# Kernel optimization log

Hardware: AMD Instinct MI355X
Metric: run time of the kernel (lower is better)

The kernel has to match this reference:

```python
import jax, jax.numpy as jnp
import numpy as np

B, T, D, H, E, TOPK = 4, 1024, 1024, 16, 8, 2
DH = D // H
FF = 4 * D
EPS = 1e-9


def setup_inputs() -> dict:
    key = jax.random.key(0)
    ks = jax.random.split(key, 8)
    s = 0.02
    return {
        "x": jax.random.normal(ks[0], (B, T, D), jnp.float32),
        "c": jax.random.normal(ks[1], (B, 1, D), jnp.float32),
        "ln1_w": jnp.ones((D,), jnp.float32),
        "w_qkv": jax.random.normal(ks[2], (3 * D, D), jnp.float32) * s,
        "w_proj": jax.random.normal(ks[3], (D, D), jnp.float32) * s,
        "ln2_w": jnp.ones((D,), jnp.float32),
        "router_w": jax.random.normal(ks[4], (E, D), jnp.float32) * s,
        "expert_w1": jax.random.normal(ks[5], (E, FF, D), jnp.float32) * s,
        "expert_w2": jax.random.normal(ks[6], (E, D, FF), jnp.float32) * s,
    }


def _layernorm(x, w):
    mu = jnp.mean(x, axis=-1, keepdims=True)
    var = jnp.mean(jnp.square(x - mu), axis=-1, keepdims=True)
    return (x - mu) * jax.lax.rsqrt(var + 1e-5) * w


def reference(x, c, ln1_w, w_qkv, w_proj, ln2_w, router_w, expert_w1, expert_w2):
    # --- causal self-attention with AdaLN-style additive conditioning ---
    h = _layernorm(x, ln1_w) + c                          # [B,T,D]
    qkv = jnp.einsum('btd,ed->bte', h, w_qkv)             # [B,T,3D]
    q, k, v = jnp.split(qkv, 3, axis=-1)
    q = q.reshape(B, T, H, DH).transpose(0, 2, 1, 3)       # [B,H,T,dh]
    k = k.reshape(B, T, H, DH).transpose(0, 2, 1, 3)
    v = v.reshape(B, T, H, DH).transpose(0, 2, 1, 3)
    scores = jnp.einsum('bhqd,bhkd->bhqk', q, k) / jnp.sqrt(jnp.float32(DH))
    causal = jnp.tril(jnp.ones((T, T), bool))
    scores = jnp.where(causal, scores, jnp.float32(-1e30))
    attn = jax.nn.softmax(scores, axis=-1)
    o = jnp.einsum('bhqk,bhkd->bhqd', attn, v)
    o = o.transpose(0, 2, 1, 3).reshape(B, T, D)
    x = x + jnp.einsum('btd,ed->bte', o, w_proj)

    # --- pre-MoE LayerNorm (note: module overwrites x with ln_2(x)) ---
    x = _layernorm(x, ln2_w)

    # --- router (non-cond path): linear, max-shift, softmax, eps clamp, top-k ---
    logits = jnp.einsum('btd,ed->bte', x, router_w)        # [B,T,E]
    logits = logits - jnp.max(logits, axis=-1, keepdims=True)
    probs = jax.nn.softmax(logits, axis=-1)
    probs = jnp.clip(probs + EPS, EPS, 1.0 - EPS)
    _, top_idx = jax.lax.top_k(probs, TOPK)                # [B,T,k]
    mask = jnp.sum(jax.nn.one_hot(top_idx, E, dtype=probs.dtype), axis=-2)  # [B,T,E]
    router_probs = mask * probs
    router_probs = router_probs / jnp.sum(router_probs, axis=-1, keepdims=True)

    # --- experts: GPT MLP per expert (fc -> GELU -> proj), combine by probs ---
    # Dense-compute form is mathematically identical: router_probs is 0 for
    # non-selected experts, so masked gather/scatter == weighted dense sum.
    hid = jax.nn.gelu(jnp.einsum('btd,efd->btef', x, expert_w1), approximate=False)
    expert_out = jnp.einsum('btef,edf->bted', hid, expert_w2)  # [B,T,E,D]
    next_states = jnp.einsum('bted,bte->btd', expert_out, router_probs)

    return x + next_states
```

## Files before the change

kernel.cpp:

```cpp
#include <hip/hip_runtime.h>
#include <cstdint>
#include <cstddef>


#define AS1 __attribute__((address_space(1)))
#define AS3 __attribute__((address_space(3)))

typedef unsigned short u16;
typedef __attribute__((ext_vector_type(8))) short short8;
typedef __attribute__((ext_vector_type(4))) float f32x4;

constexpr int Bc = 4, Tc = 1024, Dc = 1024, Hc = 16, Ec = 8, FFc = 4096;
constexpr int Mtok = Bc * Tc;

constexpr size_t PS_WQKV = (size_t)3 * Dc * Dc;
constexpr size_t PS_WPROJ = (size_t)Dc * Dc;
constexpr size_t PS_H = (size_t)Mtok * Dc;

__device__ __forceinline__ u16 f2bf(float f) {
  unsigned u = __float_as_uint(f);
  u += 0x7fffu + ((u >> 16) & 1u);
  return (u16)(u >> 16);
}
__device__ __forceinline__ float bf2f(u16 v) { return __uint_as_float(((unsigned)v) << 16); }
__device__ __forceinline__ float gelu_f(float v) {
  return 0.5f * v * (1.0f + erff(v * 0.70710678118654752440f));
}

__global__ __launch_bounds__(256) void cvt_bf16_kernel(const float* __restrict__ in,
                                                       u16* __restrict__ out, int n4) {
  int i = blockIdx.x * 256 + threadIdx.x;
  if (i >= n4) return;
  float4 v = reinterpret_cast<const float4*>(in)[i];
  uint2 o;
  o.x = (unsigned)f2bf(v.x) | ((unsigned)f2bf(v.y) << 16);
  o.y = (unsigned)f2bf(v.z) | ((unsigned)f2bf(v.w) << 16);
  reinterpret_cast<uint2*>(out)[i] = o;
}

__global__ __launch_bounds__(256) void split3_kernel(const float* __restrict__ in,
                                                     u16* __restrict__ out,
                                                     size_t ps, int n4) {
  int i = blockIdx.x * 256 + threadIdx.x;
  if (i >= n4) return;
  float4 v = reinterpret_cast<const float4*>(in)[i];
  float a[4] = {v.x, v.y, v.z, v.w};
  unsigned h[4], md[4], lo[4];
#pragma unroll
  for (int j = 0; j < 4; ++j) {
    u16 hh = f2bf(a[j]); float r = a[j] - bf2f(hh);
    u16 mm = f2bf(r);    float r2 = r - bf2f(mm);
    u16 ll = f2bf(r2);
    h[j] = hh; md[j] = mm; lo[j] = ll;
  }
  uint2 o0, o1, o2;
  o0.x = h[0] | (h[1] << 16);  o0.y = h[2] | (h[3] << 16);
  o1.x = md[0] | (md[1] << 16); o1.y = md[2] | (md[3] << 16);
  o2.x = lo[0] | (lo[1] << 16); o2.y = lo[2] | (lo[3] << 16);
  const size_t base = (size_t)i * 4;
  *(uint2*)&out[base] = o0;
  *(uint2*)&out[ps + base] = o1;
  *(uint2*)&out[2 * ps + base] = o2;
}

__global__ __launch_bounds__(256) void ln1_kernel(const float* __restrict__ x,
                                                  const float* __restrict__ w,
                                                  const float* __restrict__ c,
                                                  u16* __restrict__ hp) {
  const int row = blockIdx.x, tid = threadIdx.x;
  const int b = row >> 10;
  const float4 v = reinterpret_cast<const float4*>(x + (size_t)row * Dc)[tid];
  __shared__ float red[256];
  red[tid] = v.x + v.y + v.z + v.w;
  __syncthreads();
  for (int s = 128; s > 0; s >>= 1) { if (tid < s) red[tid] += red[tid + s]; __syncthreads(); }
  const float mu = red[0] * (1.0f / Dc);
  __syncthreads();
  const float dx = v.x - mu, dy = v.y - mu, dz = v.z - mu, dw = v.w - mu;
  red[tid] = dx * dx + dy * dy + dz * dz + dw * dw;
  __syncthreads();
  for (int s = 128; s > 0; s >>= 1) { if (tid < s) red[tid] += red[tid + s]; __syncthreads(); }
  const float rs = rsqrtf(red[0] * (1.0f / Dc) + 1e-5f);
  const float4 wv = reinterpret_cast<const float4*>(w)[tid];
  const float4 cv = reinterpret_cast<const float4*>(c + (size_t)b * Dc)[tid];
  float a[4];
  a[0] = dx * rs * wv.x + cv.x; a[1] = dy * rs * wv.y + cv.y;
  a[2] = dz * rs * wv.z + cv.z; a[3] = dw * rs * wv.w + cv.w;
  unsigned h[4], md[4], lo[4];
#pragma unroll
  for (int j = 0; j < 4; ++j) {
    u16 hh = f2bf(a[j]); float r = a[j] - bf2f(hh);
    u16 mm = f2bf(r);    float r2 = r - bf2f(mm);
    u16 ll = f2bf(r2);
    h[j] = hh; md[j] = mm; lo[j] = ll;
  }
  uint2 o0, o1, o2;
  o0.x = h[0] | (h[1] << 16);  o0.y = h[2] | (h[3] << 16);
  o1.x = md[0] | (md[1] << 16); o1.y = md[2] | (md[3] << 16);
  o2.x = lo[0] | (lo[1] << 16); o2.y = lo[2] | (lo[3] << 16);
  const size_t base = (size_t)row * Dc + tid * 4;
  *(uint2*)&hp[base] = o0;
  *(uint2*)&hp[PS_H + base] = o1;
  *(uint2*)&hp[2 * PS_H + base] = o2;
}

__global__ __launch_bounds__(256) void ln2_kernel(const float* __restrict__ xin,
                                                  const float* __restrict__ w,
                                                  float* __restrict__ xf,
                                                  u16* __restrict__ xb) {
  const int row = blockIdx.x, tid = threadIdx.x;
  const float4 v = reinterpret_cast<const float4*>(xin + (size_t)row * Dc)[tid];
  __shared__ float red[256];
  red[tid] = v.x + v.y + v.z + v.w;
  __syncthreads();
  for (int s = 128; s > 0; s >>= 1) { if (tid < s) red[tid] += red[tid + s]; __syncthreads(); }
  const float mu = red[0] * (1.0f / Dc);
  __syncthreads();
  const float dx = v.x - mu, dy = v.y - mu, dz = v.z - mu, dw = v.w - mu;
  red[tid] = dx * dx + dy * dy + dz * dz + dw * dw;
  __syncthreads();
  for (int s = 128; s > 0; s >>= 1) { if (tid < s) red[tid] += red[tid + s]; __syncthreads(); }
  const float rs = rsqrtf(red[0] * (1.0f / Dc) + 1e-5f);
  const float4 wv = reinterpret_cast<const float4*>(w)[tid];
  float4 ov;
  ov.x = dx * rs * wv.x; ov.y = dy * rs * wv.y; ov.z = dz * rs * wv.z; ov.w = dw * rs * wv.w;
  reinterpret_cast<float4*>(xf + (size_t)row * Dc)[tid] = ov;
  uint2 o;
  o.x = (unsigned)f2bf(ov.x) | ((unsigned)f2bf(ov.y) << 16);
  o.y = (unsigned)f2bf(ov.z) | ((unsigned)f2bf(ov.w) << 16);
  reinterpret_cast<uint2*>(xb + (size_t)row * Dc)[tid] = o;
}

__device__ __forceinline__ void gemm_mfma_core(const u16* a0, const u16* a1,
                                               const u16* b0, const u16* b1,
                                               int K, u16* As, u16* Bs, f32x4 acc[4][4]) {
  const int tid = threadIdx.x;
  const int lane = tid & 63;
  const int wave = tid >> 6;
  const int wm = (wave & 1) * 64;
  const int wn = (wave >> 1) * 64;
  const int frow = lane & 15;
  const int fk = (lane >> 4) * 8;
  int aoff[4], boff[4];
#pragma unroll
  for (int t = 0; t < 4; ++t) {
    aoff[t] = (wm + t * 16 + frow) * 32 + fk;
    boff[t] = (wn + t * 16 + frow) * 32 + fk;
  }
  const int lds0 = tid * 8;
  for (int k0 = 0; k0 < K; k0 += 32) {
    __builtin_amdgcn_global_load_lds((AS1 void*)a0, (AS3 void*)(As + lds0), 16, 0, 0);
    __builtin_amdgcn_global_load_lds((AS1 void*)a1, (AS3 void*)(As + 2048 + lds0), 16, 0, 0);
    __builtin_amdgcn_global_load_lds((AS1 void*)b0, (AS3 void*)(Bs + lds0), 16, 0, 0);
    __builtin_amdgcn_global_load_lds((AS1 void*)b1, (AS3 void*)(Bs + 2048 + lds0), 16, 0, 0);
    a0 += 32; a1 += 32; b0 += 32; b1 += 32;
    __syncthreads();
    short8 af[4], bfr[4];
#pragma unroll
    for (int t = 0; t < 4; ++t) af[t] = *(const short8*)(As + aoff[t]);
#pragma unroll
    for (int t = 0; t < 4; ++t) bfr[t] = *(const short8*)(Bs + boff[t]);
#pragma unroll
    for (int mt = 0; mt < 4; ++mt)
#pragma unroll
      for (int nt = 0; nt < 4; ++nt)
        acc[mt][nt] = __builtin_amdgcn_mfma_f32_16x16x32_bf16(af[mt], bfr[nt], acc[mt][nt], 0, 0, 0);
    __syncthreads();
  }
}

__device__ __forceinline__ void gemm_split_core(const u16* A0, const u16* A1, size_t Aps,
                                                const u16* B0, const u16* B1, size_t Bps,
                                                int K, u16* As, u16* Bs, f32x4 acc[4][4]) {
  const int PA[6] = {0, 0, 1, 1, 0, 2};
  const int PB[6] = {0, 1, 0, 1, 2, 0};
  for (int t6 = 0; t6 < 6; ++t6) {
    gemm_mfma_core(A0 + PA[t6] * Aps, A1 + PA[t6] * Aps,
                   B0 + PB[t6] * Bps, B1 + PB[t6] * Bps, K, As, Bs, acc);
  }
}

__global__ __launch_bounds__(256) void gemm_qkv_kernel(const u16* __restrict__ A,
                                                       const u16* __restrict__ Bw,
                                                       float* __restrict__ Cout) {
  __shared__ u16 As[128 * 32], Bs[128 * 32];
  const int bn = blockIdx.x, bm = blockIdx.y, tid = threadIdx.x;
  const int r = tid >> 2, kk = (tid & 3) * 8;
  const u16* a0 = A + (size_t)(bm * 128 + r) * 1024 + kk;
  const u16* a1 = a0 + (size_t)64 * 1024;
  const u16* b0 = Bw + (size_t)(bn * 128 + r) * 1024 + kk;
  const u16* b1 = b0 + (size_t)64 * 1024;
  f32x4 acc[4][4] = {};
  gemm_split_core(a0, a1, PS_H, b0, b1, PS_WQKV, 1024, As, Bs, acc);
  const int lane = tid & 63, wave = tid >> 6;
  const int wm = (wave & 1) * 64, wn = (wave >> 1) * 64;
  const int col = lane & 15, rb = (lane >> 4) * 4;
#pragma unroll
  for (int mt = 0; mt < 4; ++mt)
#pragma unroll
    for (int rr = 0; rr < 4; ++rr) {
      const int m = bm * 128 + wm + mt * 16 + rb + rr;
#pragma unroll
      for (int nt = 0; nt < 4; ++nt) {
        const int n = bn * 128 + wn + nt * 16 + col;
        Cout[(size_t)m * 3072 + n] = acc[mt][nt][rr];
      }
    }
}

__global__ __launch_bounds__(256) void gemm_proj_kernel(const u16* __restrict__ A,
                                                        const u16* __restrict__ Bw,
                                                        const float* __restrict__ xres,
                                                        float* __restrict__ xmid) {
  __shared__ u16 As[128 * 32], Bs[128 * 32];
  const int bn = blockIdx.x, bm = blockIdx.y, tid = threadIdx.x;
  const int r = tid >> 2, kk = (tid & 3) * 8;
  const u16* a0 = A + (size_t)(bm * 128 + r) * 1024 + kk;
  const u16* a1 = a0 + (size_t)64 * 1024;
  const u16* b0 = Bw + (size_t)(bn * 128 + r) * 1024 + kk;
  const u16* b1 = b0 + (size_t)64 * 1024;
  f32x4 acc[4][4] = {};
  gemm_split_core(a0, a1, PS_H, b0, b1, PS_WPROJ, 1024, As, Bs, acc);
  const int lane = tid & 63, wave = tid >> 6;
  const int wm = (wave & 1) * 64, wn = (wave >> 1) * 64;
  const int col = lane & 15, rb = (lane >> 4) * 4;
#pragma unroll
  for (int mt = 0; mt < 4; ++mt)
#pragma unroll
    for (int rr = 0; rr < 4; ++rr) {
      const int m = bm * 128 + wm + mt * 16 + rb + rr;
#pragma unroll
      for (int nt = 0; nt < 4; ++nt) {
        const int n = bn * 128 + wn + nt * 16 + col;
        xmid[(size_t)m * 1024 + n] = xres[(size_t)m * 1024 + n] + acc[mt][nt][rr];
      }
    }
}

__global__ __launch_bounds__(256, 3) void attn_mfma_kernel(const float* __restrict__ qkv,
                                                           float* __restrict__ obuf) {
  constexpr int KS = 72;
  constexpr int PSt = 68;
  __shared__ u16 Kh[64 * KS], Klo[64 * KS];
  __shared__ u16 Vh[64 * KS], Vlo[64 * KS];
  __shared__ u16 Ph[4][16 * PSt], Pl[4][16 * PSt];

  const int tid = threadIdx.x, lane = tid & 63, w = tid >> 6;
  const int lr = lane & 15, g = lane >> 4;
  const int bh = blockIdx.y, b = bh >> 4, h = bh & 15;
  const int blk = blockIdx.x;
  const int qrow = blk * 64 + w * 16 + lr;

  short8 qh[2], ql[2];
  {
    const float* qp = qkv + (size_t)(b * Tc + qrow) * 3072 + h * 64 + g * 8;
    const float4 f0 = *(const float4*)(qp);
    const float4 f1 = *(const float4*)(qp + 4);
    const float4 f2 = *(const float4*)(qp + 32);
    const float4 f3 = *(const float4*)(qp + 36);
    const float qq[16] = {f0.x, f0.y, f0.z, f0.w, f1.x, f1.y, f1.z, f1.w,
                          f2.x, f2.y, f2.z, f2.w, f3.x, f3.y, f3.z, f3.w};
#pragma unroll
    for (int s = 0; s < 2; ++s)
#pragma unroll
      for (int j = 0; j < 8; ++j) {
        const float v = qq[s * 8 + j] * 0.125f;
        const u16 hi = f2bf(v);
        qh[s][j] = (short)hi;
        ql[s][j] = (short)f2bf(v - bf2f(hi));
      }
  }

  const int tkl = (tid & 31) * 2;
  const int td0 = (tid >> 5) * 8;
  const float* kgb = qkv + (size_t)b * Tc * 3072 + 1024 + h * 64;
  const float* vgb = kgb + 1024;

  f32x4 oacc[4] = {};
  float mrun = -1e30f, lrun = 0.f;

  for (int c = 0; c <= blk; ++c) {
    const int k0 = c * 64;
    __syncthreads();
    {
      const float* kr0 = kgb + (size_t)(k0 + tkl) * 3072 + td0;
      const float* kr1 = kr0 + 3072;
      const float* vr0 = vgb + (size_t)(k0 + tkl) * 3072 + td0;
      const float* vr1 = vr0 + 3072;
      const float4 ka0 = *(const float4*)kr0, ka1 = *(const float4*)(kr0 + 4);
      const float4 kb0 = *(const float4*)kr1, kb1 = *(const float4*)(kr1 + 4);
      const float4 va0 = *(const float4*)vr0, va1 = *(const float4*)(vr0 + 4);
      const float4 vb0 = *(const float4*)vr1, vb1 = *(const float4*)(vr1 + 4);
      const float ka[8] = {ka0.x, ka0.y, ka0.z, ka0.w, ka1.x, ka1.y, ka1.z, ka1.w};
      const float kb[8] = {kb0.x, kb0.y, kb0.z, kb0.w, kb1.x, kb1.y, kb1.z, kb1.w};
      const float va[8] = {va0.x, va0.y, va0.z, va0.w, va1.x, va1.y, va1.z, va1.w};
      const float vb[8] = {vb0.x, vb0.y, vb0.z, vb0.w, vb1.x, vb1.y, vb1.z, vb1.w};
      short8 kh0, kl0, kh1, kl1;
#pragma unroll
      for (int j = 0; j < 8; ++j) {
        const u16 h0 = f2bf(ka[j]); kh0[j] = (short)h0; kl0[j] = (short)f2bf(ka[j] - bf2f(h0));
        const u16 h1 = f2bf(kb[j]); kh1[j] = (short)h1; kl1[j] = (short)f2bf(kb[j] - bf2f(h1));
      }
      *(short8*)(Kh + tkl * KS + td0) = kh0;
      *(short8*)(Kh + (tkl + 1) * KS + td0) = kh1;
      *(short8*)(Klo + tkl * KS + td0) = kl0;
      *(short8*)(Klo + (tkl + 1) * KS + td0) = kl1;
#pragma unroll
      for (int i = 0; i < 8; ++i) {
        const u16 h0 = f2bf(va[i]); const u16 l0 = f2bf(va[i] - bf2f(h0));
        const u16 h1 = f2bf(vb[i]); const u16 l1 = f2bf(vb[i] - bf2f(h1));
        *(unsigned*)(Vh + (td0 + i) * KS + tkl) = (unsigned)h0 | ((unsigned)h1 << 16);
        *(unsigned*)(Vlo + (td0 + i) * KS + tkl) = (unsigned)l0 | ((unsigned)l1 << 16);
      }
    }
    __syncthreads();

    f32x4 sacc[4] = {};
#pragma unroll
    for (int kt = 0; kt < 4; ++kt) {
      const u16* kap = Kh + (kt * 16 + lr) * KS + g * 8;
      const u16* klp = Klo + (kt * 16 + lr) * KS + g * 8;
      const short8 ah0 = *(const short8*)kap;
      const short8 ah1 = *(const short8*)(kap + 32);
      const short8 al0 = *(const short8*)klp;
      const short8 al1 = *(const short8*)(klp + 32);
      sacc[kt] = __builtin_amdgcn_mfma_f32_16x16x32_bf16(ah0, qh[0], sacc[kt], 0, 0, 0);
      sacc[kt] = __builtin_amdgcn_mfma_f32_16x16x32_bf16(al0, qh[0], sacc[kt], 0, 0, 0);
      sacc[kt] = __builtin_amdgcn_mfma_f32_16x16x32_bf16(ah0, ql[0], sacc[kt], 0, 0, 0);
      sacc[kt] = __builtin_amdgcn_mfma_f32_16x16x32_bf16(ah1, qh[1], sacc[kt], 0, 0, 0);
      sacc[kt] = __builtin_amdgcn_mfma_f32_16x16x32_bf16(al1, qh[1], sacc[kt], 0, 0, 0);
      sacc[kt] = __builtin_amdgcn_mfma_f32_16x16x32_bf16(ah1, ql[1], sacc[kt], 0, 0, 0);
    }

    if (c == blk) {
#pragma unroll
      for (int kt = 0; kt < 4; ++kt)
#pragma unroll
        for (int r = 0; r < 4; ++r)
          if (k0 + kt * 16 + g * 4 + r > qrow) sacc[kt][r] = -1e30f;
    }

    float mt = -1e30f;
#pragma unroll
    for (int kt = 0; kt < 4; ++kt)
#pragma unroll
      for (int r = 0; r < 4; ++r) mt = fmaxf(mt, sacc[kt][r]);
    mt = fmaxf(mt, __shfl_xor(mt, 16));
    mt = fmaxf(mt, __shfl_xor(mt, 32));
    const float mnew = fmaxf(mrun, mt);
    const float alpha = __expf(mrun - mnew);
    float psum = 0.f;
    u16* php = Ph[w] + lr * PSt;
    u16* plp = Pl[w] + lr * PSt;
#pragma unroll
    for (int kt = 0; kt < 4; ++kt) {
      u16 hh[4], ll[4];
#pragma unroll
      for (int r = 0; r < 4; ++r) {
        const float p = __expf(sacc[kt][r] - mnew);
        psum += p;
        hh[r] = f2bf(p);
        ll[r] = f2bf(p - bf2f(hh[r]));
      }
      uint2 wh, wl;
      wh.x = (unsigned)hh[0] | ((unsigned)hh[1] << 16);
      wh.y = (unsigned)hh[2] | ((unsigned)hh[3] << 16);
      wl.x = (unsigned)ll[0] | ((unsigned)ll[1] << 16);
      wl.y = (unsigned)ll[2] | ((unsigned)ll[3] << 16);
      *(uint2*)(php + kt * 16 + g * 4) = wh;
      *(uint2*)(plp + kt * 16 + g * 4) = wl;
    }
    psum += __shfl_xor(psum, 16);
    psum += __shfl_xor(psum, 32);
    mrun = mnew;
    lrun = lrun * alpha + psum;
#pragma unroll
    for (int dt = 0; dt < 4; ++dt) {
      oacc[dt][0] *= alpha; oacc[dt][1] *= alpha;
      oacc[dt][2] *= alpha; oacc[dt][3] *= alpha;
    }
    __syncthreads();

    const short8 pbh0 = *(const short8*)(php + g * 8);
    const short8 pbh1 = *(const short8*)(php + 32 + g * 8);
    const short8 pbl0 = *(const short8*)(plp + g * 8);
    const short8 pbl1 = *(const short8*)(plp + 32 + g * 8);
#pragma unroll
    for (int dt = 0; dt < 4; ++dt) {
      const u16* vap = Vh + (dt * 16 + lr) * KS + g * 8;
      const u16* vlp2 = Vlo + (dt * 16 + lr) * KS + g * 8;
      const short8 vh0 = *(const short8*)vap;
      const short8 vh1 = *(const short8*)(vap + 32);
      const short8 vl0 = *(const short8*)vlp2;
      const short8 vl1 = *(const short8*)(vlp2 + 32);
      oacc[dt] = __builtin_amdgcn_mfma_f32_16x16x32_bf16(vh0, pbh0, oacc[dt], 0, 0, 0);
      oacc[dt] = __builtin_amdgcn_mfma_f32_16x16x32_bf16(vl0, pbh0, oacc[dt], 0, 0, 0);
      oacc[dt] = __builtin_amdgcn_mfma_f32_16x16x32_bf16(vh0, pbl0, oacc[dt], 0, 0, 0);
      oacc[dt] = __builtin_amdgcn_mfma_f32_16x16x32_bf16(vh1, pbh1, oacc[dt], 0, 0, 0);
      oacc[dt] = __builtin_amdgcn_mfma_f32_16x16x32_bf16(vl1, pbh1, oacc[dt], 0, 0, 0);
      oacc[dt] = __builtin_amdgcn_mfma_f32_16x16x32_bf16(vh1, pbl1, oacc[dt], 0, 0, 0);
    }
  }

  const float invl = 1.0f / lrun;
  float* ob = obuf + (size_t)(b * Tc + qrow) * 1024 + h * 64;
#pragma unroll
  for (int dt = 0; dt < 4; ++dt) {
    float4 o4;
    o4.x = oacc[dt][0] * invl; o4.y = oacc[dt][1] * invl;
    o4.z = oacc[dt][2] * invl; o4.w = oacc[dt][3] * invl;
    *(float4*)(ob + dt * 16 + g * 4) = o4;
  }
}

__global__ __launch_bounds__(256) void router_kernel(const float* __restrict__ x2,
                                                     const float* __restrict__ rw,
                                                     int* __restrict__ cnt,
                                                     int* __restrict__ tok,
                                                     float* __restrict__ wt) {
  __shared__ float xr[1024];
  __shared__ float part[8][32];
  __shared__ float lg[8];
  const int row = blockIdx.x, tid = threadIdx.x;
  reinterpret_cast<float4*>(xr)[tid] = reinterpret_cast<const float4*>(x2 + (size_t)row * Dc)[tid];
  __syncthreads();
  const int e = tid >> 5, j = tid & 31;
  float p = 0.f;
  for (int d = j; d < Dc; d += 32) p += xr[d] * rw[e * Dc + d];
  part[e][j] = p;
  __syncthreads();
  if (tid < 8) {
    float s = 0.f;
    for (int q = 0; q < 32; ++q) s += part[tid][q];
    lg[tid] = s;
  }
  __syncthreads();
  if (tid == 0) {
    int i0 = 0;
    for (int q = 1; q < 8; ++q) if (lg[q] > lg[i0]) i0 = q;
    int i1 = (i0 == 0) ? 1 : 0;
    for (int q = 0; q < 8; ++q) if (q != i0 && lg[q] > lg[i1]) i1 = q;
    float mx = lg[0];
    for (int q = 1; q < 8; ++q) mx = fmaxf(mx, lg[q]);
    float ex[8], s = 0.f;
    for (int q = 0; q < 8; ++q) { ex[q] = expf(lg[q] - mx); s += ex[q]; }
    const float inv = 1.f / s;
    float p0v = fminf(fmaxf(ex[i0] * inv + 1e-9f, 1e-9f), 1.f - 1e-9f);
    float p1v = fminf(fmaxf(ex[i1] * inv + 1e-9f, 1e-9f), 1.f - 1e-9f);
    const float sw = 1.f / (p0v + p1v);
    int p0 = atomicAdd(&cnt[i0], 1);
    tok[i0 * Mtok + p0] = row; wt[i0 * Mtok + p0] = p0v * sw;
    int p1 = atomicAdd(&cnt[i1], 1);
    tok[i1 * Mtok + p1] = row; wt[i1 * Mtok + p1] = p1v * sw;
  }
}

__global__ __launch_bounds__(256) void gemm_e1_kernel(const u16* __restrict__ x2b,
                                                      const u16* __restrict__ w1,
                                                      const int* __restrict__ cnt,
                                                      const int* __restrict__ tok,
                                                      u16* __restrict__ hid) {
  const int bn = blockIdx.x;
  const int e = blockIdx.y >> 5, it = blockIdx.y & 31;
  const int n_e = cnt[e];
  if (it * 128 >= n_e) return;
  int offs = 0;
  for (int q = 0; q < 8; ++q) offs += (q < e) ? cnt[q] : 0;
  __shared__ u16 As[128 * 32], Bs[128 * 32];
  const int tid = threadIdx.x;
  const int r = tid >> 2, kk = (tid & 3) * 8;
  const int i0 = it * 128 + r, i1 = i0 + 64;
  const int t0 = tok[e * Mtok + ((i0 < n_e) ? i0 : (n_e - 1))];
  const int t1 = tok[e * Mtok + ((i1 < n_e) ? i1 : (n_e - 1))];
  const u16* a0 = x2b + (size_t)t0 * 1024 + kk;
  const u16* a1 = x2b + (size_t)t1 * 1024 + kk;
  const u16* b0 = w1 + (size_t)e * FFc * Dc + (size_t)(bn * 128 + r) * 1024 + kk;
  const u16* b1 = b0 + (size_t)64 * 1024;
  f32x4 acc[4][4] = {};
  gemm_mfma_core(a0, a1, b0, b1, 1024, As, Bs, acc);
  const int lane = tid & 63, wave = tid >> 6;
  const int wm = (wave & 1) * 64, wn = (wave >> 1) * 64;
  const int col = lane & 15, rb = (lane >> 4) * 4;
#pragma unroll
  for (int mt = 0; mt < 4; ++mt)
#pragma unroll
    for (int rr = 0; rr < 4; ++rr) {
      const int i = it * 128 + wm + mt * 16 + rb + rr;
      if (i < n_e) {
        const size_t hrow = (size_t)(offs + i) * FFc;
#pragma unroll
        for (int nt = 0; nt < 4; ++nt) {
          const int n = bn * 128 + wn + nt * 16 + col;
          hid[hrow + n] = f2bf(gelu_f(acc[mt][nt][rr]));
        }
      }
    }
}

__global__ __launch_bounds__(256) void gemm_e2_kernel(const u16* __restrict__ hid,
                                                      const u16* __restrict__ w2,
                                                      const int* __restrict__ cnt,
                                                      const int* __restrict__ tok,
                                                      const float* __restrict__ wt,
                                                      float* __restrict__ out) {
  const int bn = blockIdx.x;
  const int e = blockIdx.y >> 5, it = blockIdx.y & 31;
  const int n_e = cnt[e];
  if (it * 128 >= n_e) return;
  int offs = 0;
  for (int q = 0; q < 8; ++q) offs += (q < e) ? cnt[q] : 0;
  __shared__ u16 As[128 * 32], Bs[128 * 32];
  const int tid = threadIdx.x;
  const int r = tid >> 2, kk = (tid & 3) * 8;
  const int i0 = it * 128 + r, i1 = i0 + 64;
  const int ri0 = offs + ((i0 < n_e) ? i0 : (n_e - 1));
  const int ri1 = offs + ((i1 < n_e) ? i1 : (n_e - 1));
  const u16* a0 = hid + (size_t)ri0 * FFc + kk;
  const u16* a1 = hid + (size_t)ri1 * FFc + kk;
  const u16* b0 = w2 + (size_t)e * Dc * FFc + (size_t)(bn * 128 + r) * FFc + kk;
  const u16* b1 = b0 + (size_t)64 * FFc;
  f32x4 acc[4][4] = {};
  gemm_mfma_core(a0, a1, b0, b1, FFc, As, Bs, acc);
  const int lane = tid & 63, wave = tid >> 6;
  const int wm = (wave & 1) * 64, wn = (wave >> 1) * 64;
  const int col = lane & 15, rb = (lane >> 4) * 4;
#pragma unroll
  for (int mt = 0; mt < 4; ++mt)
#pragma unroll
    for (int rr = 0; rr < 4; ++rr) {
      const int i = it * 128 + wm + mt * 16 + rb + rr;
      if (i < n_e) {
        const int tk = tok[e * Mtok + i];
        const float wgt = wt[e * Mtok + i];
#pragma unroll
        for (int nt = 0; nt < 4; ++nt) {
          const int n = bn * 128 + wn + nt * 16 + col;
          atomicAdd(&out[(size_t)tk * 1024 + n], wgt * acc[mt][nt][rr]);
        }
      }
    }
}

constexpr size_t OFF_WQKV3 = 0;
constexpr size_t OFF_WPROJ3 = 18874368;
constexpr size_t OFF_W1 = 25165824;
constexpr size_t OFF_W2 = 92274688;
constexpr size_t OFF_HPL = 159383552;
constexpr size_t OFF_QKV = 184549376;
constexpr size_t OFF_OF = 234881024;
constexpr size_t OFF_X2 = 251658240;
constexpr size_t OFF_CNT = 260046848;
constexpr size_t OFF_TOK = OFF_CNT + 256;
constexpr size_t OFF_WTL = OFF_TOK + (size_t)Ec * Mtok * 4;

extern "C" void kernel_launch(void* const* d_in, const int* in_sizes, int n_in,
                              void* d_out, int out_size, void* d_ws, size_t ws_size,
                              hipStream_t stream) {
  const float* x = (const float*)d_in[0];
  const float* c = (const float*)d_in[1];
  const float* ln1_w = (const float*)d_in[2];
  const float* w_qkv = (const float*)d_in[3];
  const float* w_proj = (const float*)d_in[4];
  const float* ln2_w = (const float*)d_in[5];
  const float* router_w = (const float*)d_in[6];
  const float* ew1 = (const float*)d_in[7];
  const float* ew2 = (const float*)d_in[8];
  float* out = (float*)d_out;
  char* ws = (char*)d_ws;

  u16* wqkv3 = (u16*)(ws + OFF_WQKV3);
  u16* wproj3 = (u16*)(ws + OFF_WPROJ3);
  u16* w1_bf = (u16*)(ws + OFF_W1);
  u16* w2_bf = (u16*)(ws + OFF_W2);
  u16* hpl = (u16*)(ws + OFF_HPL);
  float* qkvf = (float*)(ws + OFF_QKV);
  float* of = (float*)(ws + OFF_OF);
  u16* x2_bf = (u16*)(ws + OFF_X2);
  u16* hid_bf = (u16*)(ws + OFF_QKV);
  int* cnt = (int*)(ws + OFF_CNT);
  int* tok = (int*)(ws + OFF_TOK);
  float* wtl = (float*)(ws + OFF_WTL);

  split3_kernel<<<(3 * Dc * Dc / 4 + 255) / 256, 256, 0, stream>>>(w_qkv, wqkv3, PS_WQKV, 3 * Dc * Dc / 4);
  split3_kernel<<<(Dc * Dc / 4 + 255) / 256, 256, 0, stream>>>(w_proj, wproj3, PS_WPROJ, Dc * Dc / 4);
  {
    int n4 = Ec * FFc * Dc / 4;
    cvt_bf16_kernel<<<(n4 + 255) / 256, 256, 0, stream>>>(ew1, w1_bf, n4);
    cvt_bf16_kernel<<<(n4 + 255) / 256, 256, 0, stream>>>(ew2, w2_bf, n4);
  }
  ln1_kernel<<<Mtok, 256, 0, stream>>>(x, ln1_w, c, hpl);
  gemm_qkv_kernel<<<dim3(24, 32), 256, 0, stream>>>(hpl, wqkv3, qkvf);
  attn_mfma_kernel<<<dim3(Tc / 64, Bc * Hc), 256, 0, stream>>>(qkvf, of);
  split3_kernel<<<(Mtok * Dc / 4 + 255) / 256, 256, 0, stream>>>(of, hpl, PS_H, Mtok * Dc / 4);
  gemm_proj_kernel<<<dim3(8, 32), 256, 0, stream>>>(hpl, wproj3, x, of);
  ln2_kernel<<<Mtok, 256, 0, stream>>>(of, ln2_w, out, x2_bf);
  (void)hipMemsetAsync(cnt, 0, Ec * sizeof(int), stream);
  router_kernel<<<Mtok, 256, 0, stream>>>(out, router_w, cnt, tok, wtl);
  gemm_e1_kernel<<<dim3(32, 256), 256, 0, stream>>>(x2_bf, w1_bf, cnt, tok, hid_bf);
  gemm_e2_kernel<<<dim3(8, 256), 256, 0, stream>>>(hid_bf, w2_bf, cnt, tok, wtl, out);
}
```

Baseline: 1.153 ms.

## Replace bf16x3 split GEMMs with fp16 two-term split and swizzle LDS

The attention QKV and projection GEMMs previously emulated fp32 with a three-way bf16 split and six bf16 MFMA passes. They now use a two-way fp16 split, with the low term scaled by 4096, and three fp16 MFMA products fused into one K loop with two accumulators. This cuts split-precision passes and operand bytes. The expert GEMMs switch from bf16 to fp16, and LDS reads and writes use an XOR swizzle to reduce bank conflicts. The risk is fp16 range overflow or underflow and slightly different accuracy.

Measured after the change: 1.032 ms. 10.5% less time.

```diff
diff --git a/kernel.cpp b/kernel.cpp
--- a/kernel.cpp
+++ b/kernel.cpp
@@ -8,6 +8,7 @@
 
 typedef unsigned short u16;
 typedef __attribute__((ext_vector_type(8))) short short8;
+typedef __attribute__((ext_vector_type(8))) _Float16 half8;
 typedef __attribute__((ext_vector_type(4))) float f32x4;
 
 constexpr int Bc = 4, Tc = 1024, Dc = 1024, Hc = 16, Ec = 8, FFc = 4096;
@@ -16,6 +17,9 @@
 constexpr size_t PS_WQKV = (size_t)3 * Dc * Dc;
 constexpr size_t PS_WPROJ = (size_t)Dc * Dc;
 constexpr size_t PS_H = (size_t)Mtok * Dc;
+
+constexpr float LO_SCALE = 4096.0f;
+constexpr float LO_INV = 1.0f / 4096.0f;
 
 __device__ __forceinline__ u16 f2bf(float f) {
   unsigned u = __float_as_uint(f);
@@ -23,44 +27,49 @@
   return (u16)(u >> 16);
 }
 __device__ __forceinline__ float bf2f(u16 v) { return __uint_as_float(((unsigned)v) << 16); }
+__device__ __forceinline__ u16 f2h(float f) {
+  _Float16 h = (_Float16)f;
+  return *(u16*)&h;
+}
+__device__ __forceinline__ float h2f(u16 v) {
+  _Float16 h = *(_Float16*)&v;
+  return (float)h;
+}
 __device__ __forceinline__ float gelu_f(float v) {
   return 0.5f * v * (1.0f + erff(v * 0.70710678118654752440f));
 }
 
-__global__ __launch_bounds__(256) void cvt_bf16_kernel(const float* __restrict__ in,
+__global__ __launch_bounds__(256) void cvt_fp16_kernel(const float* __restrict__ in,
                                                        u16* __restrict__ out, int n4) {
   int i = blockIdx.x * 256 + threadIdx.x;
   if (i >= n4) return;
   float4 v = reinterpret_cast<const float4*>(in)[i];
   uint2 o;
-  o.x = (unsigned)f2bf(v.x) | ((unsigned)f2bf(v.y) << 16);
-  o.y = (unsigned)f2bf(v.z) | ((unsigned)f2bf(v.w) << 16);
+  o.x = (unsigned)f2h(v.x) | ((unsigned)f2h(v.y) << 16);
+  o.y = (unsigned)f2h(v.z) | ((unsigned)f2h(v.w) << 16);
   reinterpret_cast<uint2*>(out)[i] = o;
 }
 
-__global__ __launch_bounds__(256) void split3_kernel(const float* __restrict__ in,
-                                                     u16* __restrict__ out,
-                                                     size_t ps, int n4) {
+__global__ __launch_bounds__(256) void split2h_kernel(const float* __restrict__ in,
+                                                      u16* __restrict__ out,
+                                                      size_t ps, int n4) {
   int i = blockIdx.x * 256 + threadIdx.x;
   if (i >= n4) return;
   float4 v = reinterpret_cast<const float4*>(in)[i];
   float a[4] = {v.x, v.y, v.z, v.w};
-  unsigned h[4], md[4], lo[4];
+  unsigned h[4], lo[4];
 #pragma unroll
   for (int j = 0; j < 4; ++j) {
-    u16 hh = f2bf(a[j]); float r = a[j] - bf2f(hh);
-    u16 mm = f2bf(r);    float r2 = r - bf2f(mm);
-    u16 ll = f2bf(r2);
-    h[j] = hh; md[j] = mm; lo[j] = ll;
-  }
-  uint2 o0, o1, o2;
-  o0.x = h[0] | (h[1] << 16);  o0.y = h[2] | (h[3] << 16);
-  o1.x = md[0] | (md[1] << 16); o1.y = md[2] | (md[3] << 16);
-  o2.x = lo[0] | (lo[1] << 16); o2.y = lo[2] | (lo[3] << 16);
+    u16 hh = f2h(a[j]);
+    float r = (a[j] - h2f(hh)) * LO_SCALE;
+    h[j] = hh; lo[j] = f2h(r);
+  }
+  uint2 o0, o1;
+  o0.x = h[0] | (h[1] << 16);   o0.y = h[2] | (h[3] << 16);
+  o1.x = lo[0] | (lo[1] << 16); o1.y = lo[2] | (lo[3] << 16);
   const size_t base = (size_t)i * 4;
   *(uint2*)&out[base] = o0;
   *(uint2*)&out[ps + base] = o1;
-  *(uint2*)&out[2 * ps + base] = o2;
 }
 
 __global__ __launch_bounds__(256) void ln1_kernel(const float* __restrict__ x,
@@ -86,22 +95,19 @@
   float a[4];
   a[0] = dx * rs * wv.x + cv.x; a[1] = dy * rs * wv.y + cv.y;
   a[2] = dz * rs * wv.z + cv.z; a[3] = dw * rs * wv.w + cv.w;
-  unsigned h[4], md[4], lo[4];
+  unsigned h[4], lo[4];
 #pragma unroll
   for (int j = 0; j < 4; ++j) {
-    u16 hh = f2bf(a[j]); float r = a[j] - bf2f(hh);
-    u16 mm = f2bf(r);    float r2 = r - bf2f(mm);
-    u16 ll = f2bf(r2);
-    h[j] = hh; md[j] = mm; lo[j] = ll;
-  }
-  uint2 o0, o1, o2;
-  o0.x = h[0] | (h[1] << 16);  o0.y = h[2] | (h[3] << 16);
-  o1.x = md[0] | (md[1] << 16); o1.y = md[2] | (md[3] << 16);
-  o2.x = lo[0] | (lo[1] << 16); o2.y = lo[2] | (lo[3] << 16);
+    u16 hh = f2h(a[j]);
+    float r = (a[j] - h2f(hh)) * LO_SCALE;
+    h[j] = hh; lo[j] = f2h(r);
+  }
+  uint2 o0, o1;
+  o0.x = h[0] | (h[1] << 16);   o0.y = h[2] | (h[3] << 16);
+  o1.x = lo[0] | (lo[1] << 16); o1.y = lo[2] | (lo[3] << 16);
   const size_t base = (size_t)row * Dc + tid * 4;
   *(uint2*)&hp[base] = o0;
   *(uint2*)&hp[PS_H + base] = o1;
-  *(uint2*)&hp[2 * PS_H + base] = o2;
 }
 
 __global__ __launch_bounds__(256) void ln2_kernel(const float* __restrict__ xin,
@@ -126,26 +132,26 @@
   ov.x = dx * rs * wv.x; ov.y = dy * rs * wv.y; ov.z = dz * rs * wv.z; ov.w = dw * rs * wv.w;
   reinterpret_cast<float4*>(xf + (size_t)row * Dc)[tid] = ov;
   uint2 o;
-  o.x = (unsigned)f2bf(ov.x) | ((unsigned)f2bf(ov.y) << 16);
-  o.y = (unsigned)f2bf(ov.z) | ((unsigned)f2bf(ov.w) << 16);
+  o.x = (unsigned)f2h(ov.x) | ((unsigned)f2h(ov.y) << 16);
+  o.y = (unsigned)f2h(ov.z) | ((unsigned)f2h(ov.w) << 16);
   reinterpret_cast<uint2*>(xb + (size_t)row * Dc)[tid] = o;
 }
 
-__device__ __forceinline__ void gemm_mfma_core(const u16* a0, const u16* a1,
-                                               const u16* b0, const u16* b1,
-                                               int K, u16* As, u16* Bs, f32x4 acc[4][4]) {
+__device__ __forceinline__ void gemm_f16_core(const u16* a0, const u16* a1,
+                                              const u16* b0, const u16* b1,
+                                              int K, u16* As, u16* Bs, f32x4 acc[4][4]) {
   const int tid = threadIdx.x;
   const int lane = tid & 63;
   const int wave = tid >> 6;
   const int wm = (wave & 1) * 64;
   const int wn = (wave >> 1) * 64;
   const int frow = lane & 15;
-  const int fk = (lane >> 4) * 8;
+  const int gs = (((lane >> 4) ^ (frow & 3))) * 8;
   int aoff[4], boff[4];
 #pragma unroll
   for (int t = 0; t < 4; ++t) {
-    aoff[t] = (wm + t * 16 + frow) * 32 + fk;
-    boff[t] = (wn + t * 16 + frow) * 32 + fk;
+    aoff[t] = (wm + t * 16 + frow) * 32 + gs;
+    boff[t] = (wn + t * 16 + frow) * 32 + gs;
   }
   const int lds0 = tid * 8;
   for (int k0 = 0; k0 < K; k0 += 32) {
@@ -155,43 +161,101 @@
     __builtin_amdgcn_global_load_lds((AS1 void*)b1, (AS3 void*)(Bs + 2048 + lds0), 16, 0, 0);
     a0 += 32; a1 += 32; b0 += 32; b1 += 32;
     __syncthreads();
-    short8 af[4], bfr[4];
-#pragma unroll
-    for (int t = 0; t < 4; ++t) af[t] = *(const short8*)(As + aoff[t]);
-#pragma unroll
-    for (int t = 0; t < 4; ++t) bfr[t] = *(const short8*)(Bs + boff[t]);
+    half8 af[4], bfr[4];
+#pragma unroll
+    for (int t = 0; t < 4; ++t) af[t] = *(const half8*)(As + aoff[t]);
+#pragma unroll
+    for (int t = 0; t < 4; ++t) bfr[t] = *(const half8*)(Bs + boff[t]);
 #pragma unroll
     for (int mt = 0; mt < 4; ++mt)
 #pragma unroll
       for (int nt = 0; nt < 4; ++nt)
-        acc[mt][nt] = __builtin_amdgcn_mfma_f32_16x16x32_bf16(af[mt], bfr[nt], acc[mt][nt], 0, 0, 0);
+        acc[mt][nt] = __builtin_amdgcn_mfma_f32_16x16x32_f16(af[mt], bfr[nt], acc[mt][nt], 0, 0, 0);
     __syncthreads();
   }
 }
 
-__device__ __forceinline__ void gemm_split_core(const u16* A0, const u16* A1, size_t Aps,
-                                                const u16* B0, const u16* B1, size_t Bps,
-                                                int K, u16* As, u16* Bs, f32x4 acc[4][4]) {
-  const int PA[6] = {0, 0, 1, 1, 0, 2};
-  const int PB[6] = {0, 1, 0, 1, 2, 0};
-  for (int t6 = 0; t6 < 6; ++t6) {
-    gemm_mfma_core(A0 + PA[t6] * Aps, A1 + PA[t6] * Aps,
-                   B0 + PB[t6] * Bps, B1 + PB[t6] * Bps, K, As, Bs, acc);
+__device__ __forceinline__ void gemm_f16s2_core(const u16* ah0, const u16* ah1,
+                                                const u16* al0, const u16* al1,
+                                                const u16* bh0, const u16* bh1,
+                                                const u16* bl0, const u16* bl1,
+                                                int K, u16* S,
+                                                f32x4 acc0[4][4], f32x4 acc1[4][4]) {
+  const int tid = threadIdx.x;
+  const int lane = tid & 63;
+  const int wave = tid >> 6;
+  const int wm = (wave & 1) * 64;
+  const int wn = (wave >> 1) * 64;
+  const int frow = lane & 15;
+  const int gs = (((lane >> 4) ^ (frow & 3))) * 8;
+  int aoff[4], boff[4];
+#pragma unroll
+  for (int t = 0; t < 4; ++t) {
+    aoff[t] = (wm + t * 16 + frow) * 32 + gs;
+    boff[t] = (wn + t * 16 + frow) * 32 + gs;
+  }
+  const int lds0 = tid * 8;
+  for (int k0 = 0; k0 < K; k0 += 32) {
+    __builtin_amdgcn_global_load_lds((AS1 void*)ah0, (AS3 void*)(S + lds0), 16, 0, 0);
+    __builtin_amdgcn_global_load_lds((AS1 void*)ah1, (AS3 void*)(S + 2048 + lds0), 16, 0, 0);
+    __builtin_amdgcn_global_load_lds((AS1 void*)al0, (AS3 void*)(S + 4096 + lds0), 16, 0, 0);
+    __builtin_amdgcn_global_load_lds((AS1 void*)al1, (AS3 void*)(S + 6144 + lds0), 16, 0, 0);
+    __builtin_amdgcn_global_load_lds((AS1 void*)bh0, (AS3 void*)(S + 8192 + lds0), 16, 0, 0);
+    __builtin_amdgcn_global_load_lds((AS1 void*)bh1, (AS3 void*)(S + 10240 + lds0), 16, 0, 0);
+    __builtin_amdgcn_global_load_lds((AS1 void*)bl0, (AS3 void*)(S + 12288 + lds0), 16, 0, 0);
+    __builtin_amdgcn_global_load_lds((AS1 void*)bl1, (AS3 void*)(S + 14336 + lds0), 16, 0, 0);
+    ah0 += 32; ah1 += 32; al0 += 32; al1 += 32;
+    bh0 += 32; bh1 += 32; bl0 += 32; bl1 += 32;
+    __syncthreads();
+    half8 ahf[4], bhf[4];
+#pragma unroll
+    for (int t = 0; t < 4; ++t) {
+      ahf[t] = *(const half8*)(S + aoff[t]);
+      bhf[t] = *(const half8*)(S + 8192 + boff[t]);
+    }
+#pragma unroll
+    for (int mt = 0; mt < 4; ++mt)
+#pragma unroll
+      for (int nt = 0; nt < 4; ++nt)
+        acc0[mt][nt] = __builtin_amdgcn_mfma_f32_16x16x32_f16(ahf[mt], bhf[nt], acc0[mt][nt], 0, 0, 0);
+    {
+      half8 alf[4];
+#pragma unroll
+      for (int t = 0; t < 4; ++t) alf[t] = *(const half8*)(S + 4096 + aoff[t]);
+#pragma unroll
+      for (int mt = 0; mt < 4; ++mt)
+#pragma unroll
+        for (int nt = 0; nt < 4; ++nt)
+          acc1[mt][nt] = __builtin_amdgcn_mfma_f32_16x16x32_f16(alf[mt], bhf[nt], acc1[mt][nt], 0, 0, 0);
+    }
+    {
+      half8 blf[4];
+#pragma unroll
+      for (int t = 0; t < 4; ++t) blf[t] = *(const half8*)(S + 12288 + boff[t]);
+#pragma unroll
+      for (int mt = 0; mt < 4; ++mt)
+#pragma unroll
+        for (int nt = 0; nt < 4; ++nt)
+          acc1[mt][nt] = __builtin_amdgcn_mfma_f32_16x16x32_f16(ahf[mt], blf[nt], acc1[mt][nt], 0, 0, 0);
+    }
+    __syncthreads();
   }
 }
 
 __global__ __launch_bounds__(256) void gemm_qkv_kernel(const u16* __restrict__ A,
                                                        const u16* __restrict__ Bw,
                                                        float* __restrict__ Cout) {
-  __shared__ u16 As[128 * 32], Bs[128 * 32];
+  __shared__ u16 S[4 * 4096];
   const int bn = blockIdx.x, bm = blockIdx.y, tid = threadIdx.x;
-  const int r = tid >> 2, kk = (tid & 3) * 8;
-  const u16* a0 = A + (size_t)(bm * 128 + r) * 1024 + kk;
-  const u16* a1 = a0 + (size_t)64 * 1024;
-  const u16* b0 = Bw + (size_t)(bn * 128 + r) * 1024 + kk;
-  const u16* b1 = b0 + (size_t)64 * 1024;
-  f32x4 acc[4][4] = {};
-  gemm_split_core(a0, a1, PS_H, b0, b1, PS_WQKV, 1024, As, Bs, acc);
+  const int r = tid >> 2, kk = ((tid & 3) ^ (r & 3)) * 8;
+  const u16* ah0 = A + (size_t)(bm * 128 + r) * 1024 + kk;
+  const u16* ah1 = ah0 + (size_t)64 * 1024;
+  const u16* bh0 = Bw + (size_t)(bn * 128 + r) * 1024 + kk;
+  const u16* bh1 = bh0 + (size_t)64 * 1024;
+  f32x4 acc0[4][4] = {}, acc1[4][4] = {};
+  gemm_f16s2_core(ah0, ah1, ah0 + PS_H, ah1 + PS_H,
+                  bh0, bh1, bh0 + PS_WQKV, bh1 + PS_WQKV,
+                  1024, S, acc0, acc1);
   const int lane = tid & 63, wave = tid >> 6;
   const int wm = (wave & 1) * 64, wn = (wave >> 1) * 64;
   const int col = lane & 15, rb = (lane >> 4) * 4;
@@ -203,7 +267,7 @@
 #pragma unroll
       for (int nt = 0; nt < 4; ++nt) {
         const int n = bn * 128 + wn + nt * 16 + col;
-        Cout[(size_t)m * 3072 + n] = acc[mt][nt][rr];
+        Cout[(size_t)m * 3072 + n] = acc0[mt][nt][rr] + acc1[mt][nt][rr] * LO_INV;
       }
     }
 }
@@ -212,15 +276,17 @@
                                                         const u16* __restrict__ Bw,
                                                         const float* __restrict__ xres,
                                                         float* __restrict__ xmid) {
-  __shared__ u16 As[128 * 32], Bs[128 * 32];
+  __shared__ u16 S[4 * 4096];
   const int bn = blockIdx.x, bm = blockIdx.y, tid = threadIdx.x;
-  const int r = tid >> 2, kk = (tid & 3) * 8;
-  const u16* a0 = A + (size_t)(bm * 128 + r) * 1024 + kk;
-  const u16* a1 = a0 + (size_t)64 * 1024;
-  const u16* b0 = Bw + (size_t)(bn * 128 + r) * 1024 + kk;
-  const u16* b1 = b0 + (size_t)64 * 1024;
-  f32x4 acc[4][4] = {};
-  gemm_split_core(a0, a1, PS_H, b0, b1, PS_WPROJ, 1024, As, Bs, acc);
+  const int r = tid >> 2, kk = ((tid & 3) ^ (r & 3)) * 8;
+  const u16* ah0 = A + (size_t)(bm * 128 + r) * 1024 + kk;
+  const u16* ah1 = ah0 + (size_t)64 * 1024;
+  const u16* bh0 = Bw + (size_t)(bn * 128 + r) * 1024 + kk;
+  const u16* bh1 = bh0 + (size_t)64 * 1024;
+  f32x4 acc0[4][4] = {}, acc1[4][4] = {};
+  gemm_f16s2_core(ah0, ah1, ah0 + PS_H, ah1 + PS_H,
+                  bh0, bh1, bh0 + PS_WPROJ, bh1 + PS_WPROJ,
+                  1024, S, acc0, acc1);
   const int lane = tid & 63, wave = tid >> 6;
   const int wm = (wave & 1) * 64, wn = (wave >> 1) * 64;
   const int col = lane & 15, rb = (lane >> 4) * 4;
@@ -232,7 +298,8 @@
 #pragma unroll
       for (int nt = 0; nt < 4; ++nt) {
         const int n = bn * 128 + wn + nt * 16 + col;
-        xmid[(size_t)m * 1024 + n] = xres[(size_t)m * 1024 + n] + acc[mt][nt][rr];
+        xmid[(size_t)m * 1024 + n] =
+            xres[(size_t)m * 1024 + n] + acc0[mt][nt][rr] + acc1[mt][nt][rr] * LO_INV;
       }
     }
 }
@@ -468,7 +535,7 @@
   for (int q = 0; q < 8; ++q) offs += (q < e) ? cnt[q] : 0;
   __shared__ u16 As[128 * 32], Bs[128 * 32];
   const int tid = threadIdx.x;
-  const int r = tid >> 2, kk = (tid & 3) * 8;
+  const int r = tid >> 2, kk = ((tid & 3) ^ (r & 3)) * 8;
   const int i0 = it * 128 + r, i1 = i0 + 64;
   const int t0 = tok[e * Mtok + ((i0 < n_e) ? i0 : (n_e - 1))];
   const int t1 = tok[e * Mtok + ((i1 < n_e) ? i1 : (n_e - 1))];
@@ -477,7 +544,7 @@
   const u16* b0 = w1 + (size_t)e * FFc * Dc + (size_t)(bn * 128 + r) * 1024 + kk;
   const u16* b1 = b0 + (size_t)64 * 1024;
   f32x4 acc[4][4] = {};
-  gemm_mfma_core(a0, a1, b0, b1, 1024, As, Bs, acc);
+  gemm_f16_core(a0, a1, b0, b1, 1024, As, Bs, acc);
   const int lane = tid & 63, wave = tid >> 6;
   const int wm = (wave & 1) * 64, wn = (wave >> 1) * 64;
   const int col = lane & 15, rb = (lane >> 4) * 4;
@@ -491,7 +558,7 @@
 #pragma unroll
         for (int nt = 0; nt < 4; ++nt) {
           const int n = bn * 128 + wn + nt * 16 + col;
-          hid[hrow + n] = f2bf(gelu_f(acc[mt][nt][rr]));
+          hid[hrow + n] = f2h(gelu_f(acc[mt][nt][rr]));
         }
       }
     }
@@ -511,7 +578,7 @@
   for (int q = 0; q < 8; ++q) offs += (q < e) ? cnt[q] : 0;
   __shared__ u16 As[128 * 32], Bs[128 * 32];
   const int tid = threadIdx.x;
-  const int r = tid >> 2, kk = (tid & 3) * 8;
+  const int r = tid >> 2, kk = ((tid & 3) ^ (r & 3)) * 8;
   const int i0 = it * 128 + r, i1 = i0 + 64;
   const int ri0 = offs + ((i0 < n_e) ? i0 : (n_e - 1));
   const int ri1 = offs + ((i1 < n_e) ? i1 : (n_e - 1));
@@ -520,7 +587,7 @@
   const u16* b0 = w2 + (size_t)e * Dc * FFc + (size_t)(bn * 128 + r) * FFc + kk;
   const u16* b1 = b0 + (size_t)64 * FFc;
   f32x4 acc[4][4] = {};
-  gemm_mfma_core(a0, a1, b0, b1, FFc, As, Bs, acc);
+  gemm_f16_core(a0, a1, b0, b1, FFc, As, Bs, acc);
   const int lane = tid & 63, wave = tid >> 6;
   const int wm = (wave & 1) * 64, wn = (wave >> 1) * 64;
   const int col = lane & 15, rb = (lane >> 4) * 4;
@@ -568,34 +635,34 @@
   float* out = (float*)d_out;
   char* ws = (char*)d_ws;
 
-  u16* wqkv3 = (u16*)(ws + OFF_WQKV3);
-  u16* wproj3 = (u16*)(ws + OFF_WPROJ3);
-  u16* w1_bf = (u16*)(ws + OFF_W1);
-  u16* w2_bf = (u16*)(ws + OFF_W2);
+  u16* wqkv2 = (u16*)(ws + OFF_WQKV3);
+  u16* wproj2 = (u16*)(ws + OFF_WPROJ3);
+  u16* w1_h = (u16*)(ws + OFF_W1);
+  u16* w2_h = (u16*)(ws + OFF_W2);
   u16* hpl = (u16*)(ws + OFF_HPL);
   float* qkvf = (float*)(ws + OFF_QKV);
   float* of = (float*)(ws + OFF_OF);
-  u16* x2_bf = (u16*)(ws + OFF_X2);
-  u16* hid_bf = (u16*)(ws + OFF_QKV);
+  u16* x2_h = (u16*)(ws + OFF_X2);
+  u16* hid_h = (u16*)(ws + OFF_QKV);
   int* cnt = (int*)(ws + OFF_CNT);
   int* tok = (int*)(ws + OFF_TOK);
   float* wtl = (float*)(ws + OFF_WTL);
 
-  split3_kernel<<<(3 * Dc * Dc / 4 + 255) / 256, 256, 0, stream>>>(w_qkv, wqkv3, PS_WQKV, 3 * Dc * Dc / 4);
-  split3_kernel<<<(Dc * Dc / 4 + 255) / 256, 256, 0, stream>>>(w_proj, wproj3, PS_WPROJ, Dc * Dc / 4);
+  split2h_kernel<<<(3 * Dc * Dc / 4 + 255) / 256, 256, 0, stream>>>(w_qkv, wqkv2, PS_WQKV, 3 * Dc * Dc / 4);
+  split2h_kernel<<<(Dc * Dc / 4 + 255) / 256, 256, 0, stream>>>(w_proj, wproj2, PS_WPROJ, Dc * Dc / 4);
   {
     int n4 = Ec * FFc * Dc / 4;
-    cvt_bf16_kernel<<<(n4 + 255) / 256, 256, 0, stream>>>(ew1, w1_bf, n4);
-    cvt_bf16_kernel<<<(n4 + 255) / 256, 256, 0, stream>>>(ew2, w2_bf, n4);
+    cvt_fp16_kernel<<<(n4 + 255) / 256, 256, 0, stream>>>(ew1, w1_h, n4);
+    cvt_fp16_kernel<<<(n4 + 255) / 256, 256, 0, stream>>>(ew2, w2_h, n4);
   }
   ln1_kernel<<<Mtok, 256, 0, stream>>>(x, ln1_w, c, hpl);
-  gemm_qkv_kernel<<<dim3(24, 32), 256, 0, stream>>>(hpl, wqkv3, qkvf);
+  gemm_qkv_kernel<<<dim3(24, 32), 256, 0, stream>>>(hpl, wqkv2, qkvf);
   attn_mfma_kernel<<<dim3(Tc / 64, Bc * Hc), 256, 0, stream>>>(qkvf, of);
-  split3_kernel<<<(Mtok * Dc / 4 + 255) / 256, 256, 0, stream>>>(of, hpl, PS_H, Mtok * Dc / 4);
-  gemm_proj_kernel<<<dim3(8, 32), 256, 0, stream>>>(hpl, wproj3, x, of);
-  ln2_kernel<<<Mtok, 256, 0, stream>>>(of, ln2_w, out, x2_bf);
+  split2h_kernel<<<(Mtok * Dc / 4 + 255) / 256, 256, 0, stream>>>(of, hpl, PS_H, Mtok * Dc / 4);
+  gemm_proj_kernel<<<dim3(8, 32), 256, 0, stream>>>(hpl, wproj2, x, of);
+  ln2_kernel<<<Mtok, 256, 0, stream>>>(of, ln2_w, out, x2_h);
   (void)hipMemsetAsync(cnt, 0, Ec * sizeof(int), stream);
   router_kernel<<<Mtok, 256, 0, stream>>>(out, router_w, cnt, tok, wtl);
-  gemm_e1_kernel<<<dim3(32, 256), 256, 0, stream>>>(x2_bf, w1_bf, cnt, tok, hid_bf);
-  gemm_e2_kernel<<<dim3(8, 256), 256, 0, stream>>>(hid_bf, w2_bf, cnt, tok, wtl, out);
-}
+  gemm_e1_kernel<<<dim3(32, 256), 256, 0, stream>>>(x2_h, w1_h, cnt, tok, hid_h);
+  gemm_e2_kernel<<<dim3(8, 256), 256, 0, stream>>>(hid_h, w2_h, cnt, tok, wtl, out);
+}
```
